# Optimization experiments

Measured on AMD Instinct MI355X. Metric: run time of the kernel, lower is better.

Reference implementation:

```python
import jax, jax.numpy as jnp
import numpy as np

ALPHA = 0.9
DT = 0.1


def setup_inputs() -> dict:
    key = jax.random.key(0)
    ks = jax.random.split(key, 9)
    B, N_in, N, L, N_out, T = 256, 784, 1024, 4, 10, 100
    s = 0.05  # small init scale to keep sin() in a sensible regime
    return {
        "X": jax.random.normal(ks[0], (B, N_in), jnp.float32),
        "Wi_w": jax.random.normal(ks[1], (N, N_in), jnp.float32) * s,
        "Wi_b": jax.random.normal(ks[2], (N,), jnp.float32) * s,
        "Win_w": jax.random.normal(ks[3], (L, N, N), jnp.float32) * s,
        "Win_b": jax.random.normal(ks[4], (L, N), jnp.float32) * s,
        "Wrec_w": jax.random.normal(ks[5], (L, N, N), jnp.float32) * s,
        "Wrec_b": jax.random.normal(ks[6], (L, N), jnp.float32) * s,
        "Wo_w": jax.random.normal(ks[7], (N_out, N), jnp.float32) * s,
        "Wo_b": jax.random.normal(ks[8], (N_out,), jnp.float32) * s,
        "T": 100,
    }


def reference(X, Wi_w, Wi_b, Win_w, Win_b, Wrec_w, Wrec_b, Wo_w, Wo_b, T):
    L = Wrec_w.shape[0]
    B = X.shape[0]
    N = Wi_w.shape[0]
    # input projection computed once (as in the original: x_in outside the loop)
    x_in = X.reshape(B, -1) @ Wi_w.T + Wi_b  # [B, N]
    h0 = jnp.zeros((L, B, N), X.dtype)

    def step(h, _):
        hs = []
        # layer 0: dh = -alpha*h + sin(x_in + W_rec0 h)
        h0n = h[0] + DT * (-ALPHA * h[0] + jnp.sin(x_in + h[0] @ Wrec_w[0].T + Wrec_b[0]))
        hs.append(h0n)
        # layers 1..L-1 use the *updated* h of the layer below (matches torch loop order)
        for l in range(1, L):
            pre = hs[l - 1] @ Win_w[l].T + Win_b[l] + h[l] @ Wrec_w[l].T + Wrec_b[l]
            hs.append(h[l] + DT * (-ALPHA * h[l] + jnp.sin(pre)))
        return jnp.stack(hs), None

    hT, _ = jax.lax.scan(step, h0, None, length=T)
    return hT[-1] @ Wo_w.T + Wo_b  # [B, N_out]
```

## Files before the change

### kernel.cpp

```cpp
#include <hip/hip_runtime.h>
#include <hip/hip_fp16.h>

constexpr float ALPHA = 0.9f;
constexpr float DT    = 0.1f;
constexpr int BB   = 256;
constexpr int NIN  = 784;
constexpr int NN   = 1024;
constexpr int LL   = 4;
constexpr int NOUT = 10;
constexpr int TT   = 100;
constexpr int KXP  = 832;
constexpr int NSTAGE = TT + LL - 1;
constexpr unsigned GRIDN = 256;
constexpr unsigned GRPSZ = 32;
constexpr int NCH = 32;

typedef _Float16 f16x8 __attribute__((ext_vector_type(8)));
typedef _Float16 f16x4 __attribute__((ext_vector_type(4)));
typedef float    f32x4 __attribute__((ext_vector_type(4)));

#define GLL16(g, l) __builtin_amdgcn_global_load_lds( \
    (const __attribute__((address_space(1))) unsigned int*)(g), \
    (__attribute__((address_space(3))) unsigned int*)(l), 16, 0, 0)

#define VMCNT(n) asm volatile("s_waitcnt vmcnt(" #n ")" ::: "memory")

__global__ void wconv_kernel(const float* __restrict__ Wrec,
                             const float* __restrict__ Win,
                             _Float16* __restrict__ Wrec_h,
                             _Float16* __restrict__ Win_h) {
    size_t i = (size_t)blockIdx.x * blockDim.x + threadIdx.x;
    float4 r = ((const float4*)Wrec)[i];
    float4 n = ((const float4*)Win)[i];
    f16x4 rh = {(_Float16)r.x, (_Float16)r.y, (_Float16)r.z, (_Float16)r.w};
    f16x4 nh = {(_Float16)n.x, (_Float16)n.y, (_Float16)n.z, (_Float16)n.w};
    ((f16x4*)Wrec_h)[i] = rh;
    ((f16x4*)Win_h)[i]  = nh;
}

__global__ void prep_kernel(const float* __restrict__ X,
                            const float* __restrict__ Wi_w,
                            _Float16* __restrict__ Xh_hi, _Float16* __restrict__ Xh_lo,
                            _Float16* __restrict__ Wih_hi, _Float16* __restrict__ Wih_lo) {
    int row = blockIdx.x;
    const float* src;
    _Float16 *dhi, *dlo;
    if (row < BB) {
        src = X + (size_t)row * NIN;
        dhi = Xh_hi + (size_t)row * KXP;  dlo = Xh_lo + (size_t)row * KXP;
    } else {
        int r = row - BB;
        src = Wi_w + (size_t)r * NIN;
        dhi = Wih_hi + (size_t)r * KXP;   dlo = Wih_lo + (size_t)r * KXP;
    }
    for (int k = threadIdx.x; k < KXP; k += 256) {
        float v = (k < NIN) ? src[k] : 0.f;
        _Float16 hi = (_Float16)v;
        dhi[k] = hi;
        dlo[k] = (_Float16)(v - (float)hi);
    }
}

__global__ void bias_kernel(const float* __restrict__ Win_b,
                            const float* __restrict__ Wrec_b,
                            float* __restrict__ bc) {
    int i = blockIdx.x * 256 + threadIdx.x;
    int l = i >> 10;
    float v = Wrec_b[i];
    if (l > 0) v += Win_b[i];
    bc[i] = v;
}

__global__ __launch_bounds__(256, 1) void xin_gemm(
    const _Float16* __restrict__ Xh_hi, const _Float16* __restrict__ Xh_lo,
    const _Float16* __restrict__ Wih_hi, const _Float16* __restrict__ Wih_lo,
    const float* __restrict__ Wi_b, float* __restrict__ x_in) {
    const int b = blockIdx.x;
    const int mt = b & 1, nt = b >> 1;
    const int row0 = mt * 128, col0 = nt * 64;

    const _Float16* Alist[3] = { Xh_hi + (size_t)row0 * KXP, Xh_hi + (size_t)row0 * KXP,
                                 Xh_lo + (size_t)row0 * KXP };
    const _Float16* Blist[3] = { Wih_hi + (size_t)col0 * KXP, Wih_lo + (size_t)col0 * KXP,
                                 Wih_hi + (size_t)col0 * KXP };

    __shared__ __align__(16) _Float16 ldsA[2][128 * 64];
    __shared__ __align__(16) _Float16 ldsB[2][64 * 64];

    const int tid = threadIdx.x;
    const int w = tid >> 6, lane = tid & 63;
    const int lm = lane & 15, kg = lane >> 4;
    const int rsub = lane >> 3, cch = lane & 7;
    const int wr = w >> 1, wc = w & 1;

    f32x4 acc[4][2] = {};
    constexpr int NIT = 3 * (KXP / 64);

    auto stage = [&](int kk, int buf) {
        int p = (kk >= 26) ? 2 : (kk >= 13 ? 1 : 0);
        int kw = (kk - p * 13) * 64;
        const _Float16* Ap = Alist[p];
        const _Float16* Bp = Blist[p];
        #pragma unroll
        for (int i = 0; i < 4; ++i) {
            const _Float16* g = Ap + (size_t)((w * 4 + i) * 8 + rsub) * KXP + kw + ((cch ^ rsub) * 8);
            GLL16(g, &ldsA[buf][(w * 4 + i) * 512]);
        }
        #pragma unroll
        for (int i = 0; i < 2; ++i) {
            const _Float16* g = Bp + (size_t)((w * 2 + i) * 8 + rsub) * KXP + kw + ((cch ^ rsub) * 8);
            GLL16(g, &ldsB[buf][(w * 2 + i) * 512]);
        }
    };

    stage(0, 0);
    __syncthreads();
    for (int kk = 0; kk < NIT; ++kk) {
        int cur = kk & 1;
        if (kk + 1 < NIT) stage(kk + 1, cur ^ 1);
        const _Float16* lA = ldsA[cur];
        const _Float16* lB = ldsB[cur];
        #pragma unroll
        for (int ks = 0; ks < 2; ++ks) {
            f16x8 a[4], bf[2];
            #pragma unroll
            for (int am = 0; am < 4; ++am) {
                int r = wr * 64 + am * 16 + lm;
                a[am] = *(const f16x8*)(lA + r * 64 + ((((ks << 2) | kg) ^ (lm & 7)) * 8));
            }
            #pragma unroll
            for (int bn = 0; bn < 2; ++bn) {
                int c = wc * 32 + bn * 16 + lm;
                bf[bn] = *(const f16x8*)(lB + c * 64 + ((((ks << 2) | kg) ^ (lm & 7)) * 8));
            }
            #pragma unroll
            for (int am = 0; am < 4; ++am)
                #pragma unroll
                for (int bn = 0; bn < 2; ++bn)
                    acc[am][bn] = __builtin_amdgcn_mfma_f32_16x16x32_f16(a[am], bf[bn], acc[am][bn], 0, 0, 0);
        }
        __syncthreads();
    }

    #pragma unroll
    for (int am = 0; am < 4; ++am)
        #pragma unroll
        for (int bn = 0; bn < 2; ++bn)
            #pragma unroll
            for (int r = 0; r < 4; ++r) {
                int row = row0 + wr * 64 + am * 16 + kg * 4 + r;
                int col = col0 + wc * 32 + bn * 16 + lm;
                x_in[(size_t)row * NN + col] = acc[am][bn][r] + Wi_b[col];
            }
}

__device__ __forceinline__ void grid_bar(unsigned* base) {
    __syncthreads();
    if (threadIdx.x == 0) {
        unsigned* flag = base + 15;
        unsigned pg = __hip_atomic_fetch_add(base + (blockIdx.x & 7), 1u,
                                             __ATOMIC_ACQ_REL, __HIP_MEMORY_SCOPE_AGENT);
        if (pg == GRPSZ - 1) {
            unsigned pr = __hip_atomic_fetch_add(base + 8, 1u,
                                                 __ATOMIC_ACQ_REL, __HIP_MEMORY_SCOPE_AGENT);
            if (pr == 7)
                __hip_atomic_store(flag, 1u, __ATOMIC_RELEASE, __HIP_MEMORY_SCOPE_AGENT);
        }
        for (int it = 0; it < (1 << 20); ++it) {
            if (__hip_atomic_load(flag, __ATOMIC_RELAXED, __HIP_MEMORY_SCOPE_AGENT)) break;
            __builtin_amdgcn_s_sleep(1);
        }
        (void)__hip_atomic_load(flag, __ATOMIC_ACQUIRE, __HIP_MEMORY_SCOPE_AGENT);
    }
    __syncthreads();
}

__global__ __launch_bounds__(512, 2) void persist_kernel(
    const _Float16* __restrict__ Wrec_h,
    const _Float16* __restrict__ Win_h,
    const float* __restrict__ bc,
    const float* __restrict__ x_in,
    float* __restrict__ Hf,
    _Float16* __restrict__ Hh,
    unsigned* __restrict__ bar) {
    const int b = blockIdx.x;
    const int l  = (b & 7) >> 1;
    const int mt = b & 1;
    const int nt = b >> 3;
    const int row0 = mt * 128, col0 = nt * 32;
    const size_t HSZ = (size_t)BB * NN;

    __shared__ __align__(16) _Float16 ldsW[2][NCH][4][32][8];
    __shared__ __align__(16) _Float16 ldsA[3][8][4][16][8];

    const int tid = threadIdx.x;
    const int w = tid >> 6, lane = tid & 63;
    const int lm = lane & 15, kg = lane >> 4;

    {
        const int ng = (l > 0) ? 2 : 1;
        for (int g = 0; g < ng; ++g) {
            const _Float16* Wg = (g ? Win_h : Wrec_h) + (size_t)l * NN * NN
                                 + (size_t)col0 * NN;
            #pragma unroll
            for (int q = 0; q < 8; ++q) {
                int idx = q * 512 + tid;
                int col = idx >> 7;
                int c   = (idx >> 2) & 31;
                int sl  = idx & 3;
                f16x8 v = *(const f16x8*)(Wg + (size_t)col * NN + c * 32 + sl * 8);
                *(f16x8*)&ldsW[g][c][sl][col][0] = v;
            }
        }
    }

    float bias0 = bc[l * NN + col0 + lm];
    float bias1 = bc[l * NN + col0 + 16 + lm];
    float hreg[2][4] = {};
    float xin[2][4] = {};
    if (l == 0) {
        #pragma unroll
        for (int r = 0; r < 4; ++r) {
            int row = row0 + w * 16 + kg * 4 + r;
            xin[0][r] = x_in[(size_t)row * NN + col0 + lm];
            xin[1][r] = x_in[(size_t)row * NN + col0 + 16 + lm];
        }
    }
    __syncthreads();

    for (int s = 0; s < NSTAGE; ++s) {
        const int t = s - l;
        if (t >= 0 && t < TT) {
            const int src = t & 1, dst = src ^ 1;
            const _Float16* A0 = Hh + ((size_t)src * LL + l) * HSZ;
            const _Float16* A1 = (l > 0) ? Hh + ((size_t)dst * LL + (l - 1)) * HSZ : A0;
            f32x4 acc0 = {0.f, 0.f, 0.f, 0.f};
            f32x4 acc1 = {0.f, 0.f, 0.f, 0.f};
            const int ngem = (l > 0) ? 2 : 1;
            for (int g = 0; g < ngem; ++g) {
                const _Float16* Ap = (g ? A1 : A0)
                    + (size_t)(row0 + w * 16 + lm) * NN + kg * 8;
                #define AISS(c, buf) GLL16(Ap + (c) * 32, &ldsA[buf][w][0][0][0])
                AISS(0, 0); AISS(1, 1);
                #pragma unroll
                for (int kk = 0; kk < NCH; ++kk) {
                    if (kk + 2 < NCH) { AISS(kk + 2, (kk + 2) % 3); VMCNT(2); }
                    else if (kk + 1 < NCH) { VMCNT(1); }
                    else { VMCNT(0); }
                    f16x8 a  = *(const f16x8*)&ldsA[kk % 3][w][kg][lm][0];
                    f16x8 b0 = *(const f16x8*)&ldsW[g][kk][kg][lm][0];
                    f16x8 b1 = *(const f16x8*)&ldsW[g][kk][kg][lm + 16][0];
                    acc0 = __builtin_amdgcn_mfma_f32_16x16x32_f16(a, b0, acc0, 0, 0, 0);
                    acc1 = __builtin_amdgcn_mfma_f32_16x16x32_f16(a, b1, acc1, 0, 0, 0);
                }
                #undef AISS
            }
            _Float16* Hhd = Hh + ((size_t)dst * LL + l) * HSZ;
            #pragma unroll
            for (int r = 0; r < 4; ++r) {
                int row = row0 + w * 16 + kg * 4 + r;
                float pre0 = acc0[r] + bias0;
                float pre1 = acc1[r] + bias1;
                if (l == 0) { pre0 += xin[0][r]; pre1 += xin[1][r]; }
                float h0 = hreg[0][r];
                h0 = h0 + DT * (-ALPHA * h0 + __sinf(pre0));
                hreg[0][r] = h0;
                Hhd[(size_t)row * NN + col0 + lm] = (_Float16)h0;
                float h1 = hreg[1][r];
                h1 = h1 + DT * (-ALPHA * h1 + __sinf(pre1));
                hreg[1][r] = h1;
                Hhd[(size_t)row * NN + col0 + 16 + lm] = (_Float16)h1;
            }
        }
        if (s < NSTAGE - 1) grid_bar(bar + s * 16);
    }

    if (l == 3) {
        float* Hfl = Hf + (size_t)3 * HSZ;
        #pragma unroll
        for (int r = 0; r < 4; ++r) {
            int row = row0 + w * 16 + kg * 4 + r;
            Hfl[(size_t)row * NN + col0 + lm]      = hreg[0][r];
            Hfl[(size_t)row * NN + col0 + 16 + lm] = hreg[1][r];
        }
    }
}

__global__ __launch_bounds__(256) void out_kernel(
    const float* __restrict__ Hf, const float* __restrict__ Wo_w,
    const float* __restrict__ Wo_b, float* __restrict__ out) {
    const int r = blockIdx.x, tid = threadIdx.x;
    const int lane = tid & 63, w = tid >> 6;
    const float* h = Hf + (size_t)3 * BB * NN + (size_t)r * NN;
    float4 h4 = ((const float4*)h)[tid];
    __shared__ float red[4][16];
    #pragma unroll
    for (int jo = 0; jo < NOUT; ++jo) {
        float4 w4 = ((const float4*)(Wo_w + (size_t)jo * NN))[tid];
        float p = h4.x * w4.x + h4.y * w4.y + h4.z * w4.z + h4.w * w4.w;
        #pragma unroll
        for (int off = 32; off; off >>= 1) p += __shfl_down(p, off);
        if (lane == 0) red[w][jo] = p;
    }
    __syncthreads();
    if (tid < NOUT)
        out[r * NOUT + tid] = red[0][tid] + red[1][tid] + red[2][tid] + red[3][tid] + Wo_b[tid];
}

extern "C" void kernel_launch(void* const* d_in, const int* in_sizes, int n_in,
                              void* d_out, int out_size, void* d_ws, size_t ws_size,
                              hipStream_t stream) {
    const float* X      = (const float*)d_in[0];
    const float* Wi_w   = (const float*)d_in[1];
    const float* Wi_b   = (const float*)d_in[2];
    const float* Win_w  = (const float*)d_in[3];
    const float* Win_b  = (const float*)d_in[4];
    const float* Wrec_w = (const float*)d_in[5];
    const float* Wrec_b = (const float*)d_in[6];
    const float* Wo_w   = (const float*)d_in[7];
    const float* Wo_b   = (const float*)d_in[8];

    char* ws = (char*)d_ws;
    _Float16* Wrec_h = (_Float16*)(ws);
    _Float16* Win_h  = (_Float16*)(ws + (size_t)(8u  << 20));
    float*    Hf     = (float*)   (ws + (size_t)(16u << 20));
    _Float16* Hh     = (_Float16*)(ws + (size_t)(20u << 20));
    float*    x_in   = (float*)   (ws + (size_t)(24u << 20));
    float*    bc     = (float*)   (ws + (size_t)(25u << 20));
    _Float16* Xh_hi  = (_Float16*)(ws + (size_t)(25u << 20) + (64u << 10));
    _Float16* Xh_lo  = (_Float16*)(ws + (size_t)(25u << 20) + (576u << 10));
    unsigned* bar    = (unsigned*)(ws + (size_t)(26u << 20));
    _Float16* Wih_hi = (_Float16*)(ws + (size_t)(20u << 20));
    _Float16* Wih_lo = Wih_hi + (size_t)NN * KXP;

    wconv_kernel<<<4096, 256, 0, stream>>>(Wrec_w, Win_w, Wrec_h, Win_h);
    prep_kernel<<<BB + NN, 256, 0, stream>>>(X, Wi_w, Xh_hi, Xh_lo, Wih_hi, Wih_lo);
    bias_kernel<<<16, 256, 0, stream>>>(Win_b, Wrec_b, bc);
    xin_gemm<<<32, 256, 0, stream>>>(Xh_hi, Xh_lo, Wih_hi, Wih_lo, Wi_b, x_in);

    hipMemsetAsync(Hf, 0, (size_t)LL * BB * NN * sizeof(float), stream);
    hipMemsetAsync(Hh, 0, (size_t)2 * LL * BB * NN * sizeof(_Float16), stream);
    hipMemsetAsync(bar, 0, NSTAGE * 16 * sizeof(unsigned), stream);

    persist_kernel<<<GRIDN, 512, 0, stream>>>(Wrec_h, Win_h, bc, x_in, Hf, Hh, bar);

    out_kernel<<<BB, 256, 0, stream>>>(Hf, Wo_w, Wo_b, (float*)d_out);
}
```

Measured before the change: 2.782 ms.

## Halve persistent grid; each block covers all batch rows with register-prefetched A

The persistent kernel now launches 128 blocks instead of 256. Each block owns one layer and a 32-column tile across all 256 batch rows, so each wave computes a 32x32 tile with four MFMAs per k-step. The LDS staging of the activation operand through global_load_lds is replaced by direct global loads into a three-deep register ring. The goal is cheaper grid barriers, since there are fewer participants, and more reuse of each weight fragment, at the cost of each block doing twice the work per stage and higher register pressure.

Result: slower. 4.033 ms (+45.0%).

```diff
diff --git a/kernel.cpp b/kernel.cpp
--- a/kernel.cpp
+++ b/kernel.cpp
@@ -11,8 +11,8 @@
 constexpr int TT   = 100;
 constexpr int KXP  = 832;
 constexpr int NSTAGE = TT + LL - 1;
-constexpr unsigned GRIDN = 256;
-constexpr unsigned GRPSZ = 32;
+constexpr unsigned GRIDN = 128;
+constexpr unsigned GRPSZ = 16;
 constexpr int NCH = 32;
 
 typedef _Float16 f16x8 __attribute__((ext_vector_type(8)));
@@ -22,8 +22,6 @@
 #define GLL16(g, l) __builtin_amdgcn_global_load_lds( \
     (const __attribute__((address_space(1))) unsigned int*)(g), \
     (__attribute__((address_space(3))) unsigned int*)(l), 16, 0, 0)
-
-#define VMCNT(n) asm volatile("s_waitcnt vmcnt(" #n ")" ::: "memory")
 
 __global__ void wconv_kernel(const float* __restrict__ Wrec,
                              const float* __restrict__ Win,
@@ -183,19 +181,18 @@
     float* __restrict__ Hf,
     _Float16* __restrict__ Hh,
     unsigned* __restrict__ bar) {
-    const int b = blockIdx.x;
-    const int l  = (b & 7) >> 1;
-    const int mt = b & 1;
-    const int nt = b >> 3;
-    const int row0 = mt * 128, col0 = nt * 32;
+    const int b  = blockIdx.x;
+    const int l  = b & 3;
+    const int nt = b >> 2;
+    const int col0 = nt * 32;
     const size_t HSZ = (size_t)BB * NN;
 
     __shared__ __align__(16) _Float16 ldsW[2][NCH][4][32][8];
-    __shared__ __align__(16) _Float16 ldsA[3][8][4][16][8];
 
     const int tid = threadIdx.x;
     const int w = tid >> 6, lane = tid & 63;
     const int lm = lane & 15, kg = lane >> 4;
+    const int row0 = w * 32;
 
     {
         const int ng = (l > 0) ? 2 : 1;
@@ -216,15 +213,18 @@
 
     float bias0 = bc[l * NN + col0 + lm];
     float bias1 = bc[l * NN + col0 + 16 + lm];
-    float hreg[2][4] = {};
-    float xin[2][4] = {};
+    float hreg[2][2][4] = {};
+    float xin[2][2][4] = {};
     if (l == 0) {
         #pragma unroll
-        for (int r = 0; r < 4; ++r) {
-            int row = row0 + w * 16 + kg * 4 + r;
-            xin[0][r] = x_in[(size_t)row * NN + col0 + lm];
-            xin[1][r] = x_in[(size_t)row * NN + col0 + 16 + lm];
-        }
+        for (int am = 0; am < 2; ++am)
+            #pragma unroll
+            for (int bn = 0; bn < 2; ++bn)
+                #pragma unroll
+                for (int r = 0; r < 4; ++r) {
+                    int row = row0 + am * 16 + kg * 4 + r;
+                    xin[am][bn][r] = x_in[(size_t)row * NN + col0 + bn * 16 + lm];
+                }
     }
     __syncthreads();
 
@@ -234,43 +234,47 @@
             const int src = t & 1, dst = src ^ 1;
             const _Float16* A0 = Hh + ((size_t)src * LL + l) * HSZ;
             const _Float16* A1 = (l > 0) ? Hh + ((size_t)dst * LL + (l - 1)) * HSZ : A0;
-            f32x4 acc0 = {0.f, 0.f, 0.f, 0.f};
-            f32x4 acc1 = {0.f, 0.f, 0.f, 0.f};
-            const int ngem = (l > 0) ? 2 : 1;
-            for (int g = 0; g < ngem; ++g) {
-                const _Float16* Ap = (g ? A1 : A0)
-                    + (size_t)(row0 + w * 16 + lm) * NN + kg * 8;
-                #define AISS(c, buf) GLL16(Ap + (c) * 32, &ldsA[buf][w][0][0][0])
-                AISS(0, 0); AISS(1, 1);
+            f32x4 acc[2][2] = {};
+            #pragma unroll 2
+            for (int g = 0; g < 2; ++g) {
+                if (g == 1 && l == 0) break;
+                const _Float16* Ap = (g ? A1 : A0) + (size_t)(row0 + lm) * NN + kg * 8;
+                f16x8 a[3][2];
+                #pragma unroll
+                for (int p = 0; p < 2; ++p) {
+                    a[p][0] = *(const f16x8*)(Ap + p * 32);
+                    a[p][1] = *(const f16x8*)(Ap + (size_t)16 * NN + p * 32);
+                }
                 #pragma unroll
                 for (int kk = 0; kk < NCH; ++kk) {
-                    if (kk + 2 < NCH) { AISS(kk + 2, (kk + 2) % 3); VMCNT(2); }
-                    else if (kk + 1 < NCH) { VMCNT(1); }
-                    else { VMCNT(0); }
-                    f16x8 a  = *(const f16x8*)&ldsA[kk % 3][w][kg][lm][0];
+                    if (kk + 2 < NCH) {
+                        a[(kk + 2) % 3][0] = *(const f16x8*)(Ap + (kk + 2) * 32);
+                        a[(kk + 2) % 3][1] = *(const f16x8*)(Ap + (size_t)16 * NN + (kk + 2) * 32);
+                    }
                     f16x8 b0 = *(const f16x8*)&ldsW[g][kk][kg][lm][0];
                     f16x8 b1 = *(const f16x8*)&ldsW[g][kk][kg][lm + 16][0];
-                    acc0 = __builtin_amdgcn_mfma_f32_16x16x32_f16(a, b0, acc0, 0, 0, 0);
-                    acc1 = __builtin_amdgcn_mfma_f32_16x16x32_f16(a, b1, acc1, 0, 0, 0);
+                    acc[0][0] = __builtin_amdgcn_mfma_f32_16x16x32_f16(a[kk % 3][0], b0, acc[0][0], 0, 0, 0);
+                    acc[0][1] = __builtin_amdgcn_mfma_f32_16x16x32_f16(a[kk % 3][0], b1, acc[0][1], 0, 0, 0);
+                    acc[1][0] = __builtin_amdgcn_mfma_f32_16x16x32_f16(a[kk % 3][1], b0, acc[1][0], 0, 0, 0);
+                    acc[1][1] = __builtin_amdgcn_mfma_f32_16x16x32_f16(a[kk % 3][1], b1, acc[1][1], 0, 0, 0);
                 }
-                #undef AISS
             }
             _Float16* Hhd = Hh + ((size_t)dst * LL + l) * HSZ;
             #pragma unroll
-            for (int r = 0; r < 4; ++r) {
-                int row = row0 + w * 16 + kg * 4 + r;
-                float pre0 = acc0[r] + bias0;
-                float pre1 = acc1[r] + bias1;
-                if (l == 0) { pre0 += xin[0][r]; pre1 += xin[1][r]; }
-                float h0 = hreg[0][r];
-                h0 = h0 + DT * (-ALPHA * h0 + __sinf(pre0));
-                hreg[0][r] = h0;
-                Hhd[(size_t)row * NN + col0 + lm] = (_Float16)h0;
-                float h1 = hreg[1][r];
-                h1 = h1 + DT * (-ALPHA * h1 + __sinf(pre1));
-                hreg[1][r] = h1;
-                Hhd[(size_t)row * NN + col0 + 16 + lm] = (_Float16)h1;
-            }
+            for (int am = 0; am < 2; ++am)
+                #pragma unroll
+                for (int bn = 0; bn < 2; ++bn)
+                    #pragma unroll
+                    for (int r = 0; r < 4; ++r) {
+                        int row = row0 + am * 16 + kg * 4 + r;
+                        int col = col0 + bn * 16 + lm;
+                        float pre = acc[am][bn][r] + (bn ? bias1 : bias0);
+                        if (l == 0) pre += xin[am][bn][r];
+                        float h = hreg[am][bn][r];
+                        h = h + DT * (-ALPHA * h + __sinf(pre));
+                        hreg[am][bn][r] = h;
+                        Hhd[(size_t)row * NN + col] = (_Float16)h;
+                    }
         }
         if (s < NSTAGE - 1) grid_bar(bar + s * 16);
     }
@@ -278,11 +282,14 @@
     if (l == 3) {
         float* Hfl = Hf + (size_t)3 * HSZ;
         #pragma unroll
-        for (int r = 0; r < 4; ++r) {
-            int row = row0 + w * 16 + kg * 4 + r;
-            Hfl[(size_t)row * NN + col0 + lm]      = hreg[0][r];
-            Hfl[(size_t)row * NN + col0 + 16 + lm] = hreg[1][r];
-        }
+        for (int am = 0; am < 2; ++am)
+            #pragma unroll
+            for (int bn = 0; bn < 2; ++bn)
+                #pragma unroll
+                for (int r = 0; r < 4; ++r) {
+                    int row = row0 + am * 16 + kg * 4 + r;
+                    Hfl[(size_t)row * NN + col0 + bn * 16 + lm] = hreg[am][bn][r];
+                }
     }
 }
 
```
